# Optimization experiments

Hardware: AMD Instinct MI355X
Metric: run time of the kernel (lower is better)

The kernel has to match this reference:

```python
import jax, jax.numpy as jnp
import numpy as np

EMB_DIM = 32
UID_TGT = 200000
IID_TGT = 50000
BATCH = 128
TOPK = 50000          # hardcoded inside test_source_free branch
TARGET_LABEL = 4.0    # module-level target rating constant


def setup_inputs() -> dict:
    key = jax.random.key(0)
    k1, k2, k3, k4, k5 = jax.random.split(key, 5)
    # x: column 0 = item id (stored as float, like the torch code), cols 1: = src_rate_pre
    iid = jax.random.randint(k1, (BATCH,), 0, IID_TGT).astype(jnp.float32)
    src_rate = jax.random.normal(k2, (BATCH, EMB_DIM), dtype=jnp.float32)
    x = jnp.concatenate([iid[:, None], src_rate], axis=1)  # [B, 1+D]
    uid_weight = 0.1 * jax.random.normal(k3, (UID_TGT, EMB_DIM), dtype=jnp.float32)
    iid_weight = 0.1 * jax.random.normal(k4, (IID_TGT, EMB_DIM), dtype=jnp.float32)
    rp_weight = 0.1 * jax.random.normal(k5, (EMB_DIM, EMB_DIM), dtype=jnp.float32)
    return {"x": x, "uid_weight": uid_weight, "iid_weight": iid_weight, "rp_weight": rp_weight}


def reference(x, uid_weight, iid_weight, rp_weight):
    # === stage == 'test_source_free' ===
    iid = x[:, 0].astype(jnp.int32)                     # [B]
    iid_emb = iid_weight[iid]                           # [B, D] item embedding gather
    src_rate_pre = x[:, 1:] @ rp_weight.T               # [B, D] Linear(emb,emb,bias=False)
    # |uid_emb . src_rate - target|  (torch: [U,B]; here kept [B,U])
    predict_rate = jnp.abs(src_rate_pre @ uid_weight.T - TARGET_LABEL)  # [B, U]
    # torch: full sort ascending + take first TOPK  ==  bottom-TOPK per row
    _, topk_idx = jax.lax.top_k(-predict_rate, TOPK)    # [B, TOPK]
    # voted rating = <selected user emb, item emb>; compute all dots once,
    # then gather (same math as gathering [B,TOPK,D] embeddings and dotting).
    all_scores = iid_emb @ uid_weight.T                 # [B, U]
    voted_rating = jnp.take_along_axis(all_scores, topk_idx, axis=1)  # [B, TOPK]
    mean_rating = jnp.mean(voted_rating, axis=1)        # [B]
    return mean_rating
```

## Files before the change

kernel.cpp:

```cpp
#include <hip/hip_runtime.h>
#include <hip/hip_bf16.h>
#include <stdint.h>

#define EMB    32
#define BATCH  128
#define NU     200000
#define KSEL   50000
#define XCOLS  33
#define SLOTS  64
#define G1     512
#define G2P    512
#define G2F    256
#define HISTW  (128 * 129)

#define OFF_SPRE   0
#define OFF_IIDE   16384
#define OFF_GHIST  32768
#define OFF_BASE16 163840
#define OFF_PREFIX 164352
#define OFF_M2     164864
#define OFF_EQ     165376
#define OFF_CAND   173568
#define OFF_PART   173568
#define PART_BYTES ((size_t)G1 * HISTW * 4)

__device__ __forceinline__ float xor1(float x) {
    int r = __builtin_amdgcn_update_dpp(0, __float_as_int(x), 0xB1, 0xF, 0xF, true);
    return __int_as_float(r);
}

__global__ void prep_kernel(const float* __restrict__ x,
                            const float* __restrict__ iid_w,
                            const float* __restrict__ rp,
                            const float* __restrict__ uid,
                            float* __restrict__ s_pre,
                            float* __restrict__ iid_emb,
                            uint32_t* __restrict__ base16,
                            uint32_t* __restrict__ eq_cnt) {
    const int b = blockIdx.x;
    const int t = threadIdx.x;
    __shared__ float xr[EMB];
    if (t < EMB) xr[t] = x[b * XCOLS + 1 + t];
    if (t == 63) eq_cnt[b * 16] = 0u;
    __syncthreads();
    if (t < EMB) {
        float acc = 0.f;
        #pragma unroll
        for (int k = 0; k < EMB; ++k) acc += xr[k] * rp[t * EMB + k];
        s_pre[b * EMB + t] = acc;
    } else {
        const int d = t - EMB;
        const int iid = (int)x[b * XCOLS];
        iid_emb[b * EMB + d] = iid_w[(size_t)iid * EMB + d];
    }
    __syncthreads();
    if (t == 0) {
        float dot = 0.f;
        #pragma unroll
        for (int k = 0; k < EMB; ++k) dot += s_pre[b * EMB + k] * uid[k];
        const uint32_t bits = __float_as_uint(fabsf(dot - 4.0f));
        const uint32_t hi = bits >> 16;
        base16[b] = (hi > 128u) ? (hi - 128u) : 0u;
    }
}

__global__ void zero_kernel(uint32_t* __restrict__ p, int n) {
    int i = blockIdx.x * blockDim.x + threadIdx.x;
    if (i < n) p[i] = 0u;
}

template <bool PART>
__global__ __launch_bounds__(1024)
void sweep1_kernel(const float* __restrict__ s_pre,
                   const float* __restrict__ uid,
                   const uint32_t* __restrict__ base16,
                   uint32_t* __restrict__ gout,
                   int jchunk) {
    extern __shared__ uint32_t hist[];
    const int t  = threadIdx.x;
    const int b  = t & 127;
    const int jl = t >> 7;
    for (int i = t; i < HISTW; i += 1024) hist[i] = 0u;
    float s[EMB];
    #pragma unroll
    for (int d = 0; d < EMB; ++d) s[d] = s_pre[b * EMB + d];
    const uint32_t base = base16[b];
    __syncthreads();

    const int j0 = blockIdx.x * jchunk;
    const int jend = min(j0 + jchunk, NU);
    int j = j0 + jl;
    for (; j + 8 < jend; j += 16) {
        const int ju = __builtin_amdgcn_readfirstlane(j);
        const float* up0 = uid + (size_t)ju * EMB;
        const float* up1 = up0 + 8 * EMB;
        float d0 = 0.f, d1 = 0.f;
        #pragma unroll
        for (int k = 0; k < EMB; ++k) {
            d0 += s[k] * up0[k];
            d1 += s[k] * up1[k];
        }
        const uint32_t bits0 = __float_as_uint(fabsf(d0 - 4.0f));
        const uint32_t bits1 = __float_as_uint(fabsf(d1 - 4.0f));
        int dg0 = (int)(bits0 >> 16) - (int)base; dg0 = dg0 < 0 ? 0 : (dg0 > 255 ? 255 : dg0);
        int dg1 = (int)(bits1 >> 16) - (int)base; dg1 = dg1 < 0 ? 0 : (dg1 > 255 ? 255 : dg1);
        atomicAdd(&hist[b * 129 + (dg0 >> 1)], 1u << ((dg0 & 1) * 16));
        atomicAdd(&hist[b * 129 + (dg1 >> 1)], 1u << ((dg1 & 1) * 16));
    }
    for (; j < jend; j += 8) {
        const int ju = __builtin_amdgcn_readfirstlane(j);
        const float* up0 = uid + (size_t)ju * EMB;
        float d0 = 0.f;
        #pragma unroll
        for (int k = 0; k < EMB; ++k) d0 += s[k] * up0[k];
        const uint32_t bits0 = __float_as_uint(fabsf(d0 - 4.0f));
        int dg0 = (int)(bits0 >> 16) - (int)base; dg0 = dg0 < 0 ? 0 : (dg0 > 255 ? 255 : dg0);
        atomicAdd(&hist[b * 129 + (dg0 >> 1)], 1u << ((dg0 & 1) * 16));
    }
    __syncthreads();
    if (PART) {
        uint32_t* part = gout + (size_t)blockIdx.x * HISTW;
        for (int i = t; i < HISTW; i += 1024) part[i] = hist[i];
    } else {
        for (int i = t; i < 128 * 256; i += 1024) {
            const int r = i >> 8, d = i & 255;
            const uint32_t c = (hist[r * 129 + (d >> 1)] >> ((d & 1) * 16)) & 0xFFFFu;
            if (c) atomicAdd(&gout[i], c);
        }
    }
}

__global__ void scan1_kernel(const uint32_t* __restrict__ ghist,
                             const uint32_t* __restrict__ base16,
                             uint32_t* __restrict__ prefix16,
                             uint32_t* __restrict__ m2) {
    const int b = threadIdx.x;
    uint32_t cum = 0, before = 0;
    int c1 = 255;
    for (int d = 0; d < 256; ++d) {
        const uint32_t c = ghist[b * 256 + d];
        if (cum + c >= (uint32_t)KSEL) { c1 = d; before = cum; break; }
        cum += c;
        if (d == 255) before = cum;
    }
    prefix16[b] = base16[b] + (uint32_t)c1;
    m2[b] = (uint32_t)KSEL - before;
}

__global__ __launch_bounds__(256)
void scan1_part_kernel(const uint32_t* __restrict__ part,
                       const uint32_t* __restrict__ base16,
                       uint32_t* __restrict__ prefix16,
                       uint32_t* __restrict__ m2) {
    const int row = blockIdx.x;
    const int t = threadIdx.x;
    __shared__ uint32_t h[256];
    const int sh = (t & 1) * 16;
    const uint32_t* p = part + (size_t)row * 129 + (t >> 1);
    uint32_t a0 = 0, a1 = 0, a2 = 0, a3 = 0;
    for (int g = 0; g < G1; g += 4) {
        a0 += (p[(size_t)(g + 0) * HISTW] >> sh) & 0xFFFFu;
        a1 += (p[(size_t)(g + 1) * HISTW] >> sh) & 0xFFFFu;
        a2 += (p[(size_t)(g + 2) * HISTW] >> sh) & 0xFFFFu;
        a3 += (p[(size_t)(g + 3) * HISTW] >> sh) & 0xFFFFu;
    }
    h[t] = a0 + a1 + a2 + a3;
    __syncthreads();
    if (t == 0) {
        uint32_t cum = 0, before = 0; int c1 = 255;
        for (int d = 0; d < 256; ++d) {
            const uint32_t c = h[d];
            if (cum + c >= (uint32_t)KSEL) { c1 = d; before = cum; break; }
            cum += c;
            if (d == 255) before = cum;
        }
        prefix16[row] = base16[row] + (uint32_t)c1;
        m2[row] = (uint32_t)KSEL - before;
    }
}

__global__ __launch_bounds__(1024)
void sweep2_kernel(const float* __restrict__ s_pre,
                   const float* __restrict__ iid_emb,
                   const float* __restrict__ uid,
                   const uint32_t* __restrict__ prefix16,
                   uint32_t* __restrict__ eq_cnt,
                   float* __restrict__ sum_part,
                   uint64_t* __restrict__ cand,
                   int cap, int jchunk) {
    extern __shared__ char smem2[];
    uint64_t* lcand  = (uint64_t*)smem2;
    uint32_t* lcnt   = (uint32_t*)(smem2 + 65536);
    uint32_t* lbase  = (uint32_t*)(smem2 + 66048);
    float*    sums_b = (float*)(smem2 + 66560);
    const int t   = threadIdx.x;
    const int par = t & 1;
    const int pr  = t >> 1;
    const int b   = pr & 127;
    const int jl  = pr >> 7;
    if (t < 128) { lcnt[t] = 0u; sums_b[t] = 0.f; }
    float c[EMB];
    {
        const float4* cp4 = (const float4*)((par ? iid_emb : s_pre) + b * EMB);
        #pragma unroll
        for (int q = 0; q < 8; ++q) {
            float4 v = cp4[q];
            c[4*q+0] = v.x; c[4*q+1] = v.y; c[4*q+2] = v.z; c[4*q+3] = v.w;
        }
    }
    const uint32_t pfx = prefix16[b];
    __syncthreads();

    const int j0 = blockIdx.x * jchunk;
    const int jend = min(j0 + jchunk, NU);
    float local = 0.f;
    int j = j0 + jl;
    for (; j + 4 < jend; j += 8) {
        const int ju = __builtin_amdgcn_readfirstlane(j);
        const float* up0 = uid + (size_t)ju * EMB;
        const float* up1 = up0 + 4 * EMB;
        float a0 = 0.f, a1 = 0.f;
        #pragma unroll
        for (int k = 0; k < EMB; ++k) {
            a0 += c[k] * up0[k];
            a1 += c[k] * up1[k];
        }
        const float p0 = xor1(a0);
        const float p1 = xor1(a1);
        if (par == 0) {
            const uint32_t bits0 = __float_as_uint(fabsf(a0 - 4.0f));
            const uint32_t bits1 = __float_as_uint(fabsf(a1 - 4.0f));
            const uint32_t hi0 = bits0 >> 16, hi1 = bits1 >> 16;
            local += (hi0 < pfx) ? p0 : 0.f;
            local += (hi1 < pfx) ? p1 : 0.f;
            if (hi0 == pfx) {
                const uint32_t pos = atomicAdd(&lcnt[b], 1u);
                const uint64_t pk = ((uint64_t)bits0 << 32) | (uint32_t)j;
                if (pos < (uint32_t)SLOTS) lcand[b * SLOTS + pos] = pk;
                else {
                    const uint32_t g = atomicAdd(&eq_cnt[b * 16], 1u);
                    if (g < (uint32_t)cap) cand[(size_t)b * cap + g] = pk;
                }
            }
            if (hi1 == pfx) {
                const uint32_t pos = atomicAdd(&lcnt[b], 1u);
                const uint64_t pk = ((uint64_t)bits1 << 32) | (uint32_t)(j + 4);
                if (pos < (uint32_t)SLOTS) lcand[b * SLOTS + pos] = pk;
                else {
                    const uint32_t g = atomicAdd(&eq_cnt[b * 16], 1u);
                    if (g < (uint32_t)cap) cand[(size_t)b * cap + g] = pk;
                }
            }
        }
    }
    for (; j < jend; j += 4) {
        const int ju = __builtin_amdgcn_readfirstlane(j);
        const float* up0 = uid + (size_t)ju * EMB;
        float a0 = 0.f;
        #pragma unroll
        for (int k = 0; k < EMB; ++k) a0 += c[k] * up0[k];
        const float p0 = xor1(a0);
        if (par == 0) {
            const uint32_t bits0 = __float_as_uint(fabsf(a0 - 4.0f));
            const uint32_t hi0 = bits0 >> 16;
            local += (hi0 < pfx) ? p0 : 0.f;
            if (hi0 == pfx) {
                const uint32_t pos = atomicAdd(&lcnt[b], 1u);
                const uint64_t pk = ((uint64_t)bits0 << 32) | (uint32_t)j;
                if (pos < (uint32_t)SLOTS) lcand[b * SLOTS + pos] = pk;
                else {
                    const uint32_t g = atomicAdd(&eq_cnt[b * 16], 1u);
                    if (g < (uint32_t)cap) cand[(size_t)b * cap + g] = pk;
                }
            }
        }
    }
    if (par == 0 && local != 0.f) atomicAdd(&sums_b[b], local);
    __syncthreads();
    if (t < 128) {
        sum_part[(size_t)blockIdx.x * 128 + t] = sums_b[t];
        const uint32_t n = min(lcnt[t], (uint32_t)SLOTS);
        lbase[t] = atomicAdd(&eq_cnt[t * 16], n);
    }
    __syncthreads();
    for (int i = t; i < 128 * SLOTS; i += 1024) {
        const int bb = i >> 6;
        const int sl = i & 63;
        if (sl < (int)min(lcnt[bb], (uint32_t)SLOTS)) {
            const uint32_t p = lbase[bb] + (uint32_t)sl;
            if (p < (uint32_t)cap) cand[(size_t)bb * cap + p] = lcand[i];
        }
    }
}

__global__ __launch_bounds__(256)
void final_kernel(const float* __restrict__ iid_emb,
                  const float* __restrict__ uid,
                  const uint32_t* __restrict__ m2_,
                  const uint32_t* __restrict__ eq_cnt,
                  const float* __restrict__ sum_part,
                  const uint64_t* __restrict__ cand,
                  int cap, int g2, float* __restrict__ out) {
    const int b = blockIdx.x;
    const int t = threadIdx.x;
    __shared__ float red[256];
    __shared__ uint32_t hist[256];
    __shared__ float e[EMB];
    __shared__ uint32_t tie[128];
    __shared__ uint32_t tiecnt, sc2, sm3, sc3, sm4;
    __shared__ float sbelow;
    if (t < EMB) e[t] = iid_emb[b * EMB + t];
    if (t == 0) tiecnt = 0u;
    hist[t] = 0u;
    {
        float acc = 0.f;
        for (int g = t; g < g2; g += 256) acc += sum_part[(size_t)g * 128 + b];
        red[t] = acc;
    }
    __syncthreads();
    for (int s = 128; s > 0; s >>= 1) { if (t < s) red[t] += red[t + s]; __syncthreads(); }
    if (t == 0) sbelow = red[0];
    __syncthreads();

    const uint32_t ec = eq_cnt[b * 16];
    const int cnt = (int)(ec < (uint32_t)cap ? ec : (uint32_t)cap);
    const uint64_t* cb = cand + (size_t)b * cap;

    for (int i = t; i < cnt; i += 256) {
        const uint32_t low16 = (uint32_t)(cb[i] >> 32) & 0xFFFFu;
        atomicAdd(&hist[low16 >> 8], 1u);
    }
    __syncthreads();
    if (t == 0) {
        const uint32_t m2v = m2_[b];
        uint32_t cum = 0, before = 0; int c2 = 255;
        for (int d = 0; d < 256; ++d) {
            const uint32_t c = hist[d];
            if (cum + c >= m2v) { c2 = d; before = cum; break; }
            cum += c;
        }
        sc2 = (uint32_t)c2; sm3 = m2v - before;
    }
    __syncthreads();
    const uint32_t c2 = sc2;
    hist[t] = 0u;
    __syncthreads();

    for (int i = t; i < cnt; i += 256) {
        const uint32_t low16 = (uint32_t)(cb[i] >> 32) & 0xFFFFu;
        if ((low16 >> 8) == c2) atomicAdd(&hist[low16 & 255u], 1u);
    }
    __syncthreads();
    if (t == 0) {
        const uint32_t m3 = sm3;
        uint32_t cum = 0, before = 0; int c3 = 255;
        for (int d = 0; d < 256; ++d) {
            const uint32_t c = hist[d];
            if (cum + c >= m3) { c3 = d; before = cum; break; }
            cum += c;
        }
        sc3 = (uint32_t)c3; sm4 = m3 - before;
    }
    __syncthreads();
    const uint32_t T16 = (c2 << 8) | sc3;

    float local = 0.f;
    for (int i = t; i < cnt; i += 256) {
        const uint64_t cv = cb[i];
        const uint32_t low16 = (uint32_t)(cv >> 32) & 0xFFFFu;
        if (low16 < T16) {
            const uint32_t j = (uint32_t)cv;
            const float4* u4 = (const float4*)(uid + (size_t)j * EMB);
            float dv = 0.f;
            #pragma unroll
            for (int q = 0; q < 8; ++q) {
                float4 u = u4[q];
                dv += e[4*q+0]*u.x + e[4*q+1]*u.y + e[4*q+2]*u.z + e[4*q+3]*u.w;
            }
            local += dv;
        } else if (low16 == T16) {
            const uint32_t pos = atomicAdd(&tiecnt, 1u);
            if (pos < 128u) tie[pos] = (uint32_t)cv;
        }
    }
    red[t] = local;
    __syncthreads();
    for (int s = 128; s > 0; s >>= 1) { if (t < s) red[t] += red[t + s]; __syncthreads(); }
    if (t == 0) {
        int tc = (int)(tiecnt < 128u ? tiecnt : 128u);
        for (int i = 1; i < tc; ++i) {
            const uint32_t v = tie[i]; int k = i - 1;
            while (k >= 0 && tie[k] > v) { tie[k+1] = tie[k]; --k; }
            tie[k+1] = v;
        }
        const int m4 = (int)sm4;
        float tsum = 0.f;
        for (int i = 0; i < m4 && i < tc; ++i) {
            const uint32_t j = tie[i];
            float dv = 0.f;
            for (int d = 0; d < EMB; ++d) dv += e[d] * uid[(size_t)j * EMB + d];
            tsum += dv;
        }
        out[b] = (sbelow + red[0] + tsum) / (float)KSEL;
    }
}

extern "C" void kernel_launch(void* const* d_in, const int* in_sizes, int n_in,
                              void* d_out, int out_size, void* d_ws, size_t ws_size,
                              hipStream_t stream) {
    const float* x     = (const float*)d_in[0];
    const float* uid   = (const float*)d_in[1];
    const float* iid_w = (const float*)d_in[2];
    const float* rp    = (const float*)d_in[3];
    float* out = (float*)d_out;

    char* ws = (char*)d_ws;
    float*    s_pre    = (float*)(ws + OFF_SPRE);
    float*    iid_emb  = (float*)(ws + OFF_IIDE);
    uint32_t* ghist    = (uint32_t*)(ws + OFF_GHIST);
    uint32_t* base16   = (uint32_t*)(ws + OFF_BASE16);
    uint32_t* prefix16 = (uint32_t*)(ws + OFF_PREFIX);
    uint32_t* m2       = (uint32_t*)(ws + OFF_M2);
    uint32_t* eq_cnt   = (uint32_t*)(ws + OFF_EQ);
    uint32_t* part     = (uint32_t*)(ws + OFF_PART);

    const size_t off_cand2 = OFF_PART + PART_BYTES;
    const bool use_part = ws_size >= off_cand2 + (size_t)128 * 8 * 4096;

    uint64_t* cand;
    int cap;
    float* sum_part;
    int g2;
    if (use_part) {
        cand = (uint64_t*)(ws + off_cand2);
        long long cap_ll = ((long long)ws_size - (long long)off_cand2) / (128LL * 8LL);
        cap = (int)(cap_ll > 16384 ? 16384 : cap_ll);
        sum_part = (float*)part;
        g2 = G2P;
    } else {
        cand = (uint64_t*)(ws + OFF_CAND);
        long long cap_ll = ((long long)ws_size - OFF_CAND) / (128LL * 8LL);
        cap = (int)(cap_ll > 16384 ? 16384 : (cap_ll < 1 ? 1 : cap_ll));
        sum_part = (float*)(ws + OFF_GHIST);
        g2 = G2F;
        const int n = (OFF_CAND - OFF_GHIST) / 4;
        zero_kernel<<<(n + 255) / 256, 256, 0, stream>>>((uint32_t*)(ws + OFF_GHIST), n);
    }

    prep_kernel<<<BATCH, 64, 0, stream>>>(x, iid_w, rp, uid, s_pre, iid_emb, base16, eq_cnt);

    const int jc1 = (NU + G1 - 1) / G1;
    if (use_part) {
        sweep1_kernel<true><<<G1, 1024, HISTW * 4, stream>>>(s_pre, uid, base16, part, jc1);
        scan1_part_kernel<<<BATCH, 256, 0, stream>>>(part, base16, prefix16, m2);
    } else {
        sweep1_kernel<false><<<G1, 1024, HISTW * 4, stream>>>(s_pre, uid, base16, ghist, jc1);
        scan1_kernel<<<1, 128, 0, stream>>>(ghist, base16, prefix16, m2);
    }

    const int jc2 = (NU + g2 - 1) / g2;
    sweep2_kernel<<<g2, 1024, 65536 + 1536, stream>>>(s_pre, iid_emb, uid,
                                                      prefix16, eq_cnt, sum_part,
                                                      cand, cap, jc2);

    final_kernel<<<BATCH, 256, 0, stream>>>(iid_emb, uid, m2, eq_cnt, sum_part,
                                            cand, cap, g2, out);
}
```

Baseline: 248.4 us.

## Stage uid rows through double-buffered LDS tiles in both sweep kernels

```diff
diff --git a/kernel.cpp b/kernel.cpp
--- a/kernel.cpp
+++ b/kernel.cpp
@@ -7,11 +7,13 @@
 #define NU     200000
 #define KSEL   50000
 #define XCOLS  33
-#define SLOTS  64
+#define SLOTS  32
 #define G1     512
 #define G2P    512
 #define G2F    256
 #define HISTW  (128 * 129)
+#define T1     32
+#define T2     64
 
 #define OFF_SPRE   0
 #define OFF_IIDE   16384
@@ -27,6 +29,17 @@
 __device__ __forceinline__ float xor1(float x) {
     int r = __builtin_amdgcn_update_dpp(0, __float_as_int(x), 0xB1, 0xF, 0xF, true);
     return __int_as_float(r);
+}
+
+__device__ __forceinline__ float dotrow(const float* __restrict__ c,
+                                        const float* __restrict__ u) {
+    float d = 0.f;
+    #pragma unroll
+    for (int q = 0; q < 8; ++q) {
+        const float4 v = *(const float4*)(u + q * 4);
+        d += c[4*q+0]*v.x + c[4*q+1]*v.y + c[4*q+2]*v.z + c[4*q+3]*v.w;
+    }
+    return d;
 }
 
 __global__ void prep_kernel(const float* __restrict__ x,
@@ -76,7 +89,9 @@
                    const uint32_t* __restrict__ base16,
                    uint32_t* __restrict__ gout,
                    int jchunk) {
-    extern __shared__ uint32_t hist[];
+    extern __shared__ uint32_t smem1[];
+    uint32_t* hist = smem1;
+    float* tiles = (float*)(smem1 + HISTW);
     const int t  = threadIdx.x;
     const int b  = t & 127;
     const int jl = t >> 7;
@@ -85,39 +100,41 @@
     #pragma unroll
     for (int d = 0; d < EMB; ++d) s[d] = s_pre[b * EMB + d];
     const uint32_t base = base16[b];
-    __syncthreads();
 
     const int j0 = blockIdx.x * jchunk;
     const int jend = min(j0 + jchunk, NU);
-    int j = j0 + jl;
-    for (; j + 8 < jend; j += 16) {
-        const int ju = __builtin_amdgcn_readfirstlane(j);
-        const float* up0 = uid + (size_t)ju * EMB;
-        const float* up1 = up0 + 8 * EMB;
-        float d0 = 0.f, d1 = 0.f;
-        #pragma unroll
-        for (int k = 0; k < EMB; ++k) {
-            d0 += s[k] * up0[k];
-            d1 += s[k] * up1[k];
-        }
-        const uint32_t bits0 = __float_as_uint(fabsf(d0 - 4.0f));
-        const uint32_t bits1 = __float_as_uint(fabsf(d1 - 4.0f));
-        int dg0 = (int)(bits0 >> 16) - (int)base; dg0 = dg0 < 0 ? 0 : (dg0 > 255 ? 255 : dg0);
-        int dg1 = (int)(bits1 >> 16) - (int)base; dg1 = dg1 < 0 ? 0 : (dg1 > 255 ? 255 : dg1);
-        atomicAdd(&hist[b * 129 + (dg0 >> 1)], 1u << ((dg0 & 1) * 16));
-        atomicAdd(&hist[b * 129 + (dg1 >> 1)], 1u << ((dg1 & 1) * 16));
-    }
-    for (; j < jend; j += 8) {
-        const int ju = __builtin_amdgcn_readfirstlane(j);
-        const float* up0 = uid + (size_t)ju * EMB;
-        float d0 = 0.f;
-        #pragma unroll
-        for (int k = 0; k < EMB; ++k) d0 += s[k] * up0[k];
-        const uint32_t bits0 = __float_as_uint(fabsf(d0 - 4.0f));
-        int dg0 = (int)(bits0 >> 16) - (int)base; dg0 = dg0 < 0 ? 0 : (dg0 > 255 ? 255 : dg0);
-        atomicAdd(&hist[b * 129 + (dg0 >> 1)], 1u << ((dg0 & 1) * 16));
-    }
-    __syncthreads();
+    const int nt = (jend - j0 + T1 - 1) / T1;
+    const int srow = t >> 5;
+
+    {
+        float v = 0.f;
+        if (j0 + srow < NU) v = uid[(size_t)j0 * EMB + t];
+        tiles[t] = v;
+    }
+    __syncthreads();
+
+    for (int tt = 0; tt < nt; ++tt) {
+        const int jt = j0 + tt * T1;
+        const bool has_next = (tt + 1 < nt);
+        float vnext = 0.f;
+        if (has_next) {
+            const int jn = jt + T1;
+            if (jn + srow < NU) vnext = uid[(size_t)jn * EMB + t];
+        }
+        const float* tp = tiles + (tt & 1) * (T1 * EMB);
+        const int lim = min(T1, jend - jt);
+        for (int r = jl; r < lim; r += 8) {
+            const float d0 = dotrow(s, tp + r * EMB);
+            const uint32_t bits0 = __float_as_uint(fabsf(d0 - 4.0f));
+            int dg0 = (int)(bits0 >> 16) - (int)base;
+            dg0 = dg0 < 0 ? 0 : (dg0 > 255 ? 255 : dg0);
+            atomicAdd(&hist[b * 129 + (dg0 >> 1)], 1u << ((dg0 & 1) * 16));
+        }
+        if (has_next) {
+            tiles[((tt + 1) & 1) * (T1 * EMB) + t] = vnext;
+        }
+        __syncthreads();
+    }
     if (PART) {
         uint32_t* part = gout + (size_t)blockIdx.x * HISTW;
         for (int i = t; i < HISTW; i += 1024) part[i] = hist[i];
@@ -190,9 +207,10 @@
                    int cap, int jchunk) {
     extern __shared__ char smem2[];
     uint64_t* lcand  = (uint64_t*)smem2;
-    uint32_t* lcnt   = (uint32_t*)(smem2 + 65536);
-    uint32_t* lbase  = (uint32_t*)(smem2 + 66048);
-    float*    sums_b = (float*)(smem2 + 66560);
+    float*    tiles  = (float*)(smem2 + 32768);
+    uint32_t* lcnt   = (uint32_t*)(smem2 + 49152);
+    uint32_t* lbase  = (uint32_t*)(smem2 + 49664);
+    float*    sums_b = (float*)(smem2 + 50176);
     const int t   = threadIdx.x;
     const int par = t & 1;
     const int pr  = t >> 1;
@@ -209,71 +227,52 @@
         }
     }
     const uint32_t pfx = prefix16[b];
-    __syncthreads();
 
     const int j0 = blockIdx.x * jchunk;
     const int jend = min(j0 + jchunk, NU);
+    const int nt = (jend - j0 + T2 - 1) / T2;
+    const int srow = t >> 4;
+
+    {
+        float2 v = make_float2(0.f, 0.f);
+        if (j0 + srow < NU) v = *(const float2*)(uid + (size_t)j0 * EMB + t * 2);
+        *(float2*)(tiles + t * 2) = v;
+    }
+    __syncthreads();
+
     float local = 0.f;
-    int j = j0 + jl;
-    for (; j + 4 < jend; j += 8) {
-        const int ju = __builtin_amdgcn_readfirstlane(j);
-        const float* up0 = uid + (size_t)ju * EMB;
-        const float* up1 = up0 + 4 * EMB;
-        float a0 = 0.f, a1 = 0.f;
-        #pragma unroll
-        for (int k = 0; k < EMB; ++k) {
-            a0 += c[k] * up0[k];
-            a1 += c[k] * up1[k];
-        }
-        const float p0 = xor1(a0);
-        const float p1 = xor1(a1);
-        if (par == 0) {
-            const uint32_t bits0 = __float_as_uint(fabsf(a0 - 4.0f));
-            const uint32_t bits1 = __float_as_uint(fabsf(a1 - 4.0f));
-            const uint32_t hi0 = bits0 >> 16, hi1 = bits1 >> 16;
-            local += (hi0 < pfx) ? p0 : 0.f;
-            local += (hi1 < pfx) ? p1 : 0.f;
-            if (hi0 == pfx) {
-                const uint32_t pos = atomicAdd(&lcnt[b], 1u);
-                const uint64_t pk = ((uint64_t)bits0 << 32) | (uint32_t)j;
-                if (pos < (uint32_t)SLOTS) lcand[b * SLOTS + pos] = pk;
-                else {
-                    const uint32_t g = atomicAdd(&eq_cnt[b * 16], 1u);
-                    if (g < (uint32_t)cap) cand[(size_t)b * cap + g] = pk;
+    for (int tt = 0; tt < nt; ++tt) {
+        const int jt = j0 + tt * T2;
+        const bool has_next = (tt + 1 < nt);
+        float2 vnext = make_float2(0.f, 0.f);
+        if (has_next) {
+            const int jn = jt + T2;
+            if (jn + srow < NU) vnext = *(const float2*)(uid + (size_t)jn * EMB + t * 2);
+        }
+        const float* tp = tiles + (tt & 1) * (T2 * EMB);
+        const int lim = min(T2, jend - jt);
+        for (int r = jl; r < lim; r += 4) {
+            const float a0 = dotrow(c, tp + r * EMB);
+            const float p0 = xor1(a0);
+            if (par == 0) {
+                const uint32_t bits0 = __float_as_uint(fabsf(a0 - 4.0f));
+                const uint32_t hi0 = bits0 >> 16;
+                local += (hi0 < pfx) ? p0 : 0.f;
+                if (hi0 == pfx) {
+                    const uint32_t pos = atomicAdd(&lcnt[b], 1u);
+                    const uint64_t pk = ((uint64_t)bits0 << 32) | (uint32_t)(jt + r);
+                    if (pos < (uint32_t)SLOTS) lcand[b * SLOTS + pos] = pk;
+                    else {
+                        const uint32_t g = atomicAdd(&eq_cnt[b * 16], 1u);
+                        if (g < (uint32_t)cap) cand[(size_t)b * cap + g] = pk;
+                    }
                 }
             }
-            if (hi1 == pfx) {
-                const uint32_t pos = atomicAdd(&lcnt[b], 1u);
-                const uint64_t pk = ((uint64_t)bits1 << 32) | (uint32_t)(j + 4);
-                if (pos < (uint32_t)SLOTS) lcand[b * SLOTS + pos] = pk;
-                else {
-                    const uint32_t g = atomicAdd(&eq_cnt[b * 16], 1u);
-                    if (g < (uint32_t)cap) cand[(size_t)b * cap + g] = pk;
-                }
-            }
-        }
-    }
-    for (; j < jend; j += 4) {
-        const int ju = __builtin_amdgcn_readfirstlane(j);
-        const float* up0 = uid + (size_t)ju * EMB;
-        float a0 = 0.f;
-        #pragma unroll
-        for (int k = 0; k < EMB; ++k) a0 += c[k] * up0[k];
-        const float p0 = xor1(a0);
-        if (par == 0) {
-            const uint32_t bits0 = __float_as_uint(fabsf(a0 - 4.0f));
-            const uint32_t hi0 = bits0 >> 16;
-            local += (hi0 < pfx) ? p0 : 0.f;
-            if (hi0 == pfx) {
-                const uint32_t pos = atomicAdd(&lcnt[b], 1u);
-                const uint64_t pk = ((uint64_t)bits0 << 32) | (uint32_t)j;
-                if (pos < (uint32_t)SLOTS) lcand[b * SLOTS + pos] = pk;
-                else {
-                    const uint32_t g = atomicAdd(&eq_cnt[b * 16], 1u);
-                    if (g < (uint32_t)cap) cand[(size_t)b * cap + g] = pk;
-                }
-            }
-        }
+        }
+        if (has_next) {
+            *(float2*)(tiles + ((tt + 1) & 1) * (T2 * EMB) + t * 2) = vnext;
+        }
+        __syncthreads();
     }
     if (par == 0 && local != 0.f) atomicAdd(&sums_b[b], local);
     __syncthreads();
@@ -284,8 +283,8 @@
     }
     __syncthreads();
     for (int i = t; i < 128 * SLOTS; i += 1024) {
-        const int bb = i >> 6;
-        const int sl = i & 63;
+        const int bb = i >> 5;
+        const int sl = i & 31;
         if (sl < (int)min(lcnt[bb], (uint32_t)SLOTS)) {
             const uint32_t p = lbase[bb] + (uint32_t)sl;
             if (p < (uint32_t)cap) cand[(size_t)bb * cap + p] = lcand[i];
@@ -450,18 +449,20 @@
     prep_kernel<<<BATCH, 64, 0, stream>>>(x, iid_w, rp, uid, s_pre, iid_emb, base16, eq_cnt);
 
     const int jc1 = (NU + G1 - 1) / G1;
+    const size_t lds1 = HISTW * 4 + 2 * T1 * EMB * 4;
     if (use_part) {
-        sweep1_kernel<true><<<G1, 1024, HISTW * 4, stream>>>(s_pre, uid, base16, part, jc1);
+        sweep1_kernel<true><<<G1, 1024, lds1, stream>>>(s_pre, uid, base16, part, jc1);
         scan1_part_kernel<<<BATCH, 256, 0, stream>>>(part, base16, prefix16, m2);
     } else {
-        sweep1_kernel<false><<<G1, 1024, HISTW * 4, stream>>>(s_pre, uid, base16, ghist, jc1);
+        sweep1_kernel<false><<<G1, 1024, lds1, stream>>>(s_pre, uid, base16, ghist, jc1);
         scan1_kernel<<<1, 128, 0, stream>>>(ghist, base16, prefix16, m2);
     }
 
     const int jc2 = (NU + g2 - 1) / g2;
-    sweep2_kernel<<<g2, 1024, 65536 + 1536, stream>>>(s_pre, iid_emb, uid,
-                                                      prefix16, eq_cnt, sum_part,
-                                                      cand, cap, jc2);
+    const size_t lds2 = 32768 + 16384 + 1536;
+    sweep2_kernel<<<g2, 1024, lds2, stream>>>(s_pre, iid_emb, uid,
+                                              prefix16, eq_cnt, sum_part,
+                                              cand, cap, jc2);
 
     final_kernel<<<BATCH, 256, 0, stream>>>(iid_emb, uid, m2, eq_cnt, sum_part,
                                             cand, cap, g2, out);
```

Measured after the change: 225.3 us. 9.3% less time.
